# Optimization experiments

Hardware: AMD Instinct MI355X
Metric: run time of the kernel (lower is better)

The kernel has to match this reference:

```python
import jax, jax.numpy as jnp
import numpy as np

NEG_BIG = -9e15

def setup_inputs() -> dict:
    key = jax.random.key(0)
    k1, k2, k3, k4 = jax.random.split(key, 4)
    N, Fin, Fout = 8192, 256, 128
    x = jax.random.normal(k1, (N, Fin), dtype=jnp.float32)
    adj = jax.random.randint(k2, (N, N), 0, 2, dtype=jnp.int32)
    # xavier-uniform-like init
    limW = float(np.sqrt(6.0 / (Fin + Fout)))
    W = jax.random.uniform(k3, (Fin, Fout), minval=-limW, maxval=limW, dtype=jnp.float32)
    lima = float(np.sqrt(6.0 / (2 * Fout + 1)))
    a = jax.random.uniform(k4, (2 * Fout, 1), minval=-lima, maxval=lima, dtype=jnp.float32)
    return {"x": x, "adj": adj, "W": W, "a": a}

def reference(x, adj, W, a, alpha=0.2):
    # h: (N, Fout)
    h = x @ W
    Fout = W.shape[1]
    # Split a into source/target halves: e[i,j] = leakyrelu(h_i·a1 + h_j·a2)
    a1, a2 = a[:Fout, 0], a[Fout:, 0]
    s = h @ a1  # (N,) row (source) scores
    t = h @ a2  # (N,) col (target) scores
    e = jax.nn.leaky_relu(s[:, None] + t[None, :], negative_slope=alpha)  # (N, N)
    e = jnp.where(adj > 0, e, NEG_BIG)
    attention = jax.nn.softmax(e, axis=1)
    # dropout omitted (eval mode / training=False)
    return attention @ h
```

## Files before the change

### kernel.cpp

```cpp
#include <hip/hip_runtime.h>
#include <hip/hip_bf16.h>

typedef __attribute__((ext_vector_type(8))) short short8;
typedef __attribute__((ext_vector_type(4))) short short4v;
typedef __attribute__((ext_vector_type(4))) float f32x4;

#define NR 8192
#define LOG2E 1.4426950408889634f

__device__ __forceinline__ short f2bf(float f) {
  return __builtin_bit_cast(short, __float2bfloat16(f));
}
__device__ __forceinline__ float bf2f(short s) {
  unsigned u = ((unsigned)(unsigned short)s) << 16;
  return __builtin_bit_cast(float, u);
}

__global__ __launch_bounds__(256) void k_gemm_h(const float* __restrict__ x,
                                                const float* __restrict__ W,
                                                short* __restrict__ HT) {
  __shared__ short WT[128][136];
  const int tid = threadIdx.x;
  const int w = tid >> 6;
  const int L = tid & 63;
  const int lm = L & 15;
  const int q = L >> 4;
  const int i0 = blockIdx.x * 128;

  f32x4 acc[2][8];
#pragma unroll
  for (int mm = 0; mm < 2; ++mm)
#pragma unroll
    for (int nn = 0; nn < 8; ++nn) acc[mm][nn] = (f32x4){0.f, 0.f, 0.f, 0.f};

  for (int kc = 0; kc < 256; kc += 128) {
    if (kc) __syncthreads();
#pragma unroll
    for (int p = 0; p < 16; ++p) {
      int idx = p * 256 + tid;
      int k = idx >> 5;
      int f4 = (idx & 31) * 4;
      float4 v = *(const float4*)&W[(kc + k) * 128 + f4];
      WT[f4 + 0][k] = f2bf(v.x);
      WT[f4 + 1][k] = f2bf(v.y);
      WT[f4 + 2][k] = f2bf(v.z);
      WT[f4 + 3][k] = f2bf(v.w);
    }
    __syncthreads();
#pragma unroll
    for (int ks = 0; ks < 4; ++ks) {
      short8 afrag[2];
#pragma unroll
      for (int mm = 0; mm < 2; ++mm) {
        int row = i0 + 32 * w + 16 * mm + lm;
        const float* xp = &x[(size_t)row * 256 + kc + ks * 32 + q * 8];
        float4 xa = *(const float4*)xp;
        float4 xb = *(const float4*)(xp + 4);
        short8 af;
        af[0] = f2bf(xa.x); af[1] = f2bf(xa.y); af[2] = f2bf(xa.z); af[3] = f2bf(xa.w);
        af[4] = f2bf(xb.x); af[5] = f2bf(xb.y); af[6] = f2bf(xb.z); af[7] = f2bf(xb.w);
        afrag[mm] = af;
      }
#pragma unroll
      for (int nn = 0; nn < 8; ++nn) {
        short8 bf = *(const short8*)&WT[nn * 16 + lm][ks * 32 + q * 8];
        acc[0][nn] = __builtin_amdgcn_mfma_f32_16x16x32_bf16(afrag[0], bf, acc[0][nn], 0, 0, 0);
        acc[1][nn] = __builtin_amdgcn_mfma_f32_16x16x32_bf16(afrag[1], bf, acc[1][nn], 0, 0, 0);
      }
    }
  }
#pragma unroll
  for (int mm = 0; mm < 2; ++mm) {
    int ib = i0 + 32 * w + 16 * mm + 4 * q;
#pragma unroll
    for (int nn = 0; nn < 8; ++nn) {
      int f = nn * 16 + lm;
      short4v o;
      o[0] = f2bf(acc[mm][nn][0]);
      o[1] = f2bf(acc[mm][nn][1]);
      o[2] = f2bf(acc[mm][nn][2]);
      o[3] = f2bf(acc[mm][nn][3]);
      *(short4v*)&HT[(size_t)f * NR + ib] = o;
    }
  }
}

__global__ __launch_bounds__(256) void k_st(const short* __restrict__ HT,
                                            const float* __restrict__ a,
                                            float* __restrict__ sv,
                                            float* __restrict__ tv) {
  int i = blockIdx.x * 256 + threadIdx.x;
  float s = 0.f, t = 0.f;
#pragma unroll 4
  for (int f = 0; f < 128; ++f) {
    float h = bf2f(HT[(size_t)f * NR + i]);
    s += h * a[f];
    t += h * a[128 + f];
  }
  sv[i] = s * LOG2E;
  tv[i] = t * LOG2E;
}

__global__ __launch_bounds__(256) void k_flash(const int* __restrict__ adj,
                                               const short* __restrict__ HT,
                                               const float* __restrict__ sv,
                                               const float* __restrict__ tv,
                                               float* __restrict__ part,
                                               float* __restrict__ lpart,
                                               int S, int JR) {
  __shared__ short Ht[128][136];
  const int tid = threadIdx.x;
  const int w = tid >> 6;
  const int L = tid & 63;
  const int lm = L & 15;
  const int q = L >> 4;
  const int sp = blockIdx.x >> 6;
  const int it = blockIdx.x & 63;
  const int i0 = it * 128;

  const int row0 = i0 + 32 * w + lm;
  const int row1 = row0 + 16;
  const float s0 = sv[row0];
  const float s1 = sv[row1];

  f32x4 acc[2][8];
#pragma unroll
  for (int mm = 0; mm < 2; ++mm)
#pragma unroll
    for (int nn = 0; nn < 8; ++nn) acc[mm][nn] = (f32x4){0.f, 0.f, 0.f, 0.f};
  float l0 = 0.f, l1 = 0.f;

  const int ntiles = JR >> 7;
  for (int jt = 0; jt < ntiles; ++jt) {
    const int j0 = sp * JR + jt * 128;
    __syncthreads();
#pragma unroll
    for (int c = 0; c < 8; ++c) {
      int idx = c * 256 + tid;
      int f = idx >> 4;
      int ch = idx & 15;
      *(uint4*)&Ht[f][ch * 8] = *(const uint4*)&HT[(size_t)f * NR + j0 + ch * 8];
    }
    __syncthreads();
#pragma unroll
    for (int kk = 0; kk < 4; ++kk) {
      const int jb = j0 + kk * 32 + q * 8;
      float4 t0 = *(const float4*)&tv[jb];
      float4 t1 = *(const float4*)&tv[jb + 4];
      const int4* ap0 = (const int4*)&adj[(size_t)row0 * NR + jb];
      const int4* ap1 = (const int4*)&adj[(size_t)row1 * NR + jb];
      int4 a00 = ap0[0], a01 = ap0[1];
      int4 a10 = ap1[0], a11 = ap1[1];
      float tvl[8] = {t0.x, t0.y, t0.z, t0.w, t1.x, t1.y, t1.z, t1.w};
      int av0[8] = {a00.x, a00.y, a00.z, a00.w, a01.x, a01.y, a01.z, a01.w};
      int av1[8] = {a10.x, a10.y, a10.z, a10.w, a11.x, a11.y, a11.z, a11.w};
      short8 p0, p1;
#pragma unroll
      for (int e = 0; e < 8; ++e) {
        float v0 = s0 + tvl[e];
        float e0 = fmaxf(v0, 0.2f * v0);
        float pp0 = (av0[e] > 0) ? __builtin_amdgcn_exp2f(e0) : 0.f;
        l0 += pp0;
        p0[e] = f2bf(pp0);
        float v1 = s1 + tvl[e];
        float e1 = fmaxf(v1, 0.2f * v1);
        float pp1 = (av1[e] > 0) ? __builtin_amdgcn_exp2f(e1) : 0.f;
        l1 += pp1;
        p1[e] = f2bf(pp1);
      }
#pragma unroll
      for (int nn = 0; nn < 8; ++nn) {
        short8 bf = *(const short8*)&Ht[nn * 16 + lm][kk * 32 + q * 8];
        acc[0][nn] = __builtin_amdgcn_mfma_f32_16x16x32_bf16(p0, bf, acc[0][nn], 0, 0, 0);
        acc[1][nn] = __builtin_amdgcn_mfma_f32_16x16x32_bf16(p1, bf, acc[1][nn], 0, 0, 0);
      }
    }
  }

  float* ps = part + (size_t)sp * (NR * 128);
#pragma unroll
  for (int mm = 0; mm < 2; ++mm) {
    int ib = i0 + 32 * w + 16 * mm + 4 * q;
#pragma unroll
    for (int nn = 0; nn < 8; ++nn) {
      int f = nn * 16 + lm;
#pragma unroll
      for (int r = 0; r < 4; ++r) ps[(size_t)(ib + r) * 128 + f] = acc[mm][nn][r];
    }
  }
  l0 += __shfl_xor(l0, 16);
  l0 += __shfl_xor(l0, 32);
  l1 += __shfl_xor(l1, 16);
  l1 += __shfl_xor(l1, 32);
  if (q == 0) {
    lpart[sp * NR + row0] = l0;
    lpart[sp * NR + row1] = l1;
  }
}

__global__ __launch_bounds__(256) void k_reduce(const float* __restrict__ part,
                                                const float* __restrict__ lpart,
                                                float* __restrict__ out, int S) {
  int idx = blockIdx.x * 256 + threadIdx.x;
  int i = idx >> 7;
  float sum = 0.f;
  for (int sp = 0; sp < S; ++sp) sum += part[(size_t)sp * (NR * 128) + idx];
  float l = 0.f;
  for (int sp = 0; sp < S; ++sp) l += lpart[sp * NR + i];
  out[idx] = (l > 0.f) ? sum / l : 0.f;
}

extern "C" void kernel_launch(void* const* d_in, const int* in_sizes, int n_in,
                              void* d_out, int out_size, void* d_ws, size_t ws_size,
                              hipStream_t stream) {
  const float* x = (const float*)d_in[0];
  const int* adj = (const int*)d_in[1];
  const float* W = (const float*)d_in[2];
  const float* a = (const float*)d_in[3];
  float* out = (float*)d_out;

  char* ws = (char*)d_ws;
  short* HT = (short*)(ws + 0);
  float* sv = (float*)(ws + 2097152);
  float* tv = (float*)(ws + 2129920);
  float* lpart = (float*)(ws + 2162688);
  float* part = (float*)(ws + 2424832);

  int S = 8;
  while (S > 1 && (size_t)2424832 + (size_t)S * 4194304 > ws_size) S >>= 1;
  int JR = NR / S;

  hipLaunchKernelGGL(k_gemm_h, dim3(64), dim3(256), 0, stream, x, W, HT);
  hipLaunchKernelGGL(k_st, dim3(32), dim3(256), 0, stream, HT, a, sv, tv);
  hipLaunchKernelGGL(k_flash, dim3(64 * S), dim3(256), 0, stream, adj, HT, sv, tv,
                     part, lpart, S, JR);
  hipLaunchKernelGGL(k_reduce, dim3((NR * 128) / 256), dim3(256), 0, stream, part,
                     lpart, out, S);
}
```

Measured before the change: 466.0 us.

## Fuse score computation into GEMM, drop LDS staging in flash, widen split

The s/t score reduction moves into the h GEMM epilogue using cross-lane shuffles, which removes the separate k_st kernel. The GEMM now uses 64-row blocks so the grid is twice as large. The flash kernel stops staging H tiles in LDS behind barriers and loads B fragments straight from global/L2 in a 32-column loop, with launch bounds set for 3 blocks per SM. The split-K factor rises to 16 for more parallelism, and the reduce kernel is vectorised to float4. The trade-offs are more global-load traffic per wave for H and a larger partial buffer to reduce.

```diff
diff --git a/kernel.cpp b/kernel.cpp
--- a/kernel.cpp
+++ b/kernel.cpp
@@ -11,27 +11,24 @@
 __device__ __forceinline__ short f2bf(float f) {
   return __builtin_bit_cast(short, __float2bfloat16(f));
 }
-__device__ __forceinline__ float bf2f(short s) {
-  unsigned u = ((unsigned)(unsigned short)s) << 16;
-  return __builtin_bit_cast(float, u);
-}
 
 __global__ __launch_bounds__(256) void k_gemm_h(const float* __restrict__ x,
                                                 const float* __restrict__ W,
-                                                short* __restrict__ HT) {
+                                                const float* __restrict__ a,
+                                                short* __restrict__ HT,
+                                                float* __restrict__ sv,
+                                                float* __restrict__ tv) {
   __shared__ short WT[128][136];
   const int tid = threadIdx.x;
   const int w = tid >> 6;
   const int L = tid & 63;
   const int lm = L & 15;
   const int q = L >> 4;
-  const int i0 = blockIdx.x * 128;
-
-  f32x4 acc[2][8];
-#pragma unroll
-  for (int mm = 0; mm < 2; ++mm)
-#pragma unroll
-    for (int nn = 0; nn < 8; ++nn) acc[mm][nn] = (f32x4){0.f, 0.f, 0.f, 0.f};
+  const int i0 = blockIdx.x * 64;
+
+  f32x4 acc[8];
+#pragma unroll
+  for (int nn = 0; nn < 8; ++nn) acc[nn] = (f32x4){0.f, 0.f, 0.f, 0.f};
 
   for (int kc = 0; kc < 256; kc += 128) {
     if (kc) __syncthreads();
@@ -49,66 +46,69 @@
     __syncthreads();
 #pragma unroll
     for (int ks = 0; ks < 4; ++ks) {
-      short8 afrag[2];
-#pragma unroll
-      for (int mm = 0; mm < 2; ++mm) {
-        int row = i0 + 32 * w + 16 * mm + lm;
-        const float* xp = &x[(size_t)row * 256 + kc + ks * 32 + q * 8];
-        float4 xa = *(const float4*)xp;
-        float4 xb = *(const float4*)(xp + 4);
-        short8 af;
-        af[0] = f2bf(xa.x); af[1] = f2bf(xa.y); af[2] = f2bf(xa.z); af[3] = f2bf(xa.w);
-        af[4] = f2bf(xb.x); af[5] = f2bf(xb.y); af[6] = f2bf(xb.z); af[7] = f2bf(xb.w);
-        afrag[mm] = af;
-      }
+      int row = i0 + 16 * w + lm;
+      const float* xp = &x[(size_t)row * 256 + kc + ks * 32 + q * 8];
+      float4 xa = *(const float4*)xp;
+      float4 xb = *(const float4*)(xp + 4);
+      short8 af;
+      af[0] = f2bf(xa.x); af[1] = f2bf(xa.y); af[2] = f2bf(xa.z); af[3] = f2bf(xa.w);
+      af[4] = f2bf(xb.x); af[5] = f2bf(xb.y); af[6] = f2bf(xb.z); af[7] = f2bf(xb.w);
 #pragma unroll
       for (int nn = 0; nn < 8; ++nn) {
         short8 bf = *(const short8*)&WT[nn * 16 + lm][ks * 32 + q * 8];
-        acc[0][nn] = __builtin_amdgcn_mfma_f32_16x16x32_bf16(afrag[0], bf, acc[0][nn], 0, 0, 0);
-        acc[1][nn] = __builtin_amdgcn_mfma_f32_16x16x32_bf16(afrag[1], bf, acc[1][nn], 0, 0, 0);
+        acc[nn] = __builtin_amdgcn_mfma_f32_16x16x32_bf16(af, bf, acc[nn], 0, 0, 0);
       }
     }
   }
-#pragma unroll
-  for (int mm = 0; mm < 2; ++mm) {
-    int ib = i0 + 32 * w + 16 * mm + 4 * q;
-#pragma unroll
-    for (int nn = 0; nn < 8; ++nn) {
-      int f = nn * 16 + lm;
-      short4v o;
-      o[0] = f2bf(acc[mm][nn][0]);
-      o[1] = f2bf(acc[mm][nn][1]);
-      o[2] = f2bf(acc[mm][nn][2]);
-      o[3] = f2bf(acc[mm][nn][3]);
-      *(short4v*)&HT[(size_t)f * NR + ib] = o;
-    }
-  }
-}
-
-__global__ __launch_bounds__(256) void k_st(const short* __restrict__ HT,
-                                            const float* __restrict__ a,
-                                            float* __restrict__ sv,
-                                            float* __restrict__ tv) {
-  int i = blockIdx.x * 256 + threadIdx.x;
-  float s = 0.f, t = 0.f;
-#pragma unroll 4
-  for (int f = 0; f < 128; ++f) {
-    float h = bf2f(HT[(size_t)f * NR + i]);
-    s += h * a[f];
-    t += h * a[128 + f];
-  }
-  sv[i] = s * LOG2E;
-  tv[i] = t * LOG2E;
-}
-
-__global__ __launch_bounds__(256) void k_flash(const int* __restrict__ adj,
-                                               const short* __restrict__ HT,
-                                               const float* __restrict__ sv,
-                                               const float* __restrict__ tv,
-                                               float* __restrict__ part,
-                                               float* __restrict__ lpart,
-                                               int S, int JR) {
-  __shared__ short Ht[128][136];
+
+  const int ib = i0 + 16 * w + 4 * q;
+  float a1v[8], a2v[8];
+#pragma unroll
+  for (int nn = 0; nn < 8; ++nn) {
+    a1v[nn] = a[nn * 16 + lm];
+    a2v[nn] = a[128 + nn * 16 + lm];
+  }
+  float sr[4] = {0.f, 0.f, 0.f, 0.f};
+  float tr[4] = {0.f, 0.f, 0.f, 0.f};
+#pragma unroll
+  for (int nn = 0; nn < 8; ++nn) {
+    int f = nn * 16 + lm;
+    short4v o;
+    o[0] = f2bf(acc[nn][0]);
+    o[1] = f2bf(acc[nn][1]);
+    o[2] = f2bf(acc[nn][2]);
+    o[3] = f2bf(acc[nn][3]);
+    *(short4v*)&HT[(size_t)f * NR + ib] = o;
+#pragma unroll
+    for (int r = 0; r < 4; ++r) {
+      sr[r] += acc[nn][r] * a1v[nn];
+      tr[r] += acc[nn][r] * a2v[nn];
+    }
+  }
+#pragma unroll
+  for (int d = 1; d < 16; d <<= 1) {
+#pragma unroll
+    for (int r = 0; r < 4; ++r) {
+      sr[r] += __shfl_xor(sr[r], d);
+      tr[r] += __shfl_xor(tr[r], d);
+    }
+  }
+  if (lm == 0) {
+#pragma unroll
+    for (int r = 0; r < 4; ++r) {
+      sv[ib + r] = sr[r] * LOG2E;
+      tv[ib + r] = tr[r] * LOG2E;
+    }
+  }
+}
+
+__global__ __launch_bounds__(256, 3) void k_flash(const int* __restrict__ adj,
+                                                  const short* __restrict__ HT,
+                                                  const float* __restrict__ sv,
+                                                  const float* __restrict__ tv,
+                                                  float* __restrict__ part,
+                                                  float* __restrict__ lpart,
+                                                  int S) {
   const int tid = threadIdx.x;
   const int w = tid >> 6;
   const int L = tid & 63;
@@ -122,6 +122,8 @@
   const int row1 = row0 + 16;
   const float s0 = sv[row0];
   const float s1 = sv[row1];
+  const size_t ar0 = (size_t)row0 * NR;
+  const size_t ar1 = (size_t)row1 * NR;
 
   f32x4 acc[2][8];
 #pragma unroll
@@ -130,50 +132,45 @@
     for (int nn = 0; nn < 8; ++nn) acc[mm][nn] = (f32x4){0.f, 0.f, 0.f, 0.f};
   float l0 = 0.f, l1 = 0.f;
 
-  const int ntiles = JR >> 7;
-  for (int jt = 0; jt < ntiles; ++jt) {
-    const int j0 = sp * JR + jt * 128;
-    __syncthreads();
-#pragma unroll
-    for (int c = 0; c < 8; ++c) {
-      int idx = c * 256 + tid;
-      int f = idx >> 4;
-      int ch = idx & 15;
-      *(uint4*)&Ht[f][ch * 8] = *(const uint4*)&HT[(size_t)f * NR + j0 + ch * 8];
-    }
-    __syncthreads();
-#pragma unroll
-    for (int kk = 0; kk < 4; ++kk) {
-      const int jb = j0 + kk * 32 + q * 8;
-      float4 t0 = *(const float4*)&tv[jb];
-      float4 t1 = *(const float4*)&tv[jb + 4];
-      const int4* ap0 = (const int4*)&adj[(size_t)row0 * NR + jb];
-      const int4* ap1 = (const int4*)&adj[(size_t)row1 * NR + jb];
-      int4 a00 = ap0[0], a01 = ap0[1];
-      int4 a10 = ap1[0], a11 = ap1[1];
-      float tvl[8] = {t0.x, t0.y, t0.z, t0.w, t1.x, t1.y, t1.z, t1.w};
-      int av0[8] = {a00.x, a00.y, a00.z, a00.w, a01.x, a01.y, a01.z, a01.w};
-      int av1[8] = {a10.x, a10.y, a10.z, a10.w, a11.x, a11.y, a11.z, a11.w};
-      short8 p0, p1;
-#pragma unroll
-      for (int e = 0; e < 8; ++e) {
-        float v0 = s0 + tvl[e];
-        float e0 = fmaxf(v0, 0.2f * v0);
-        float pp0 = (av0[e] > 0) ? __builtin_amdgcn_exp2f(e0) : 0.f;
-        l0 += pp0;
-        p0[e] = f2bf(pp0);
-        float v1 = s1 + tvl[e];
-        float e1 = fmaxf(v1, 0.2f * v1);
-        float pp1 = (av1[e] > 0) ? __builtin_amdgcn_exp2f(e1) : 0.f;
-        l1 += pp1;
-        p1[e] = f2bf(pp1);
-      }
-#pragma unroll
-      for (int nn = 0; nn < 8; ++nn) {
-        short8 bf = *(const short8*)&Ht[nn * 16 + lm][kk * 32 + q * 8];
-        acc[0][nn] = __builtin_amdgcn_mfma_f32_16x16x32_bf16(p0, bf, acc[0][nn], 0, 0, 0);
-        acc[1][nn] = __builtin_amdgcn_mfma_f32_16x16x32_bf16(p1, bf, acc[1][nn], 0, 0, 0);
-      }
+  const int JR = NR / S;
+  const int j0 = sp * JR;
+  const int niter = JR >> 5;
+
+#pragma unroll 2
+  for (int jk = 0; jk < niter; ++jk) {
+    const int jb = j0 + (jk << 5) + q * 8;
+    float4 t0 = *(const float4*)&tv[jb];
+    float4 t1 = *(const float4*)&tv[jb + 4];
+    int4 a00 = *(const int4*)&adj[ar0 + jb];
+    int4 a01 = *(const int4*)&adj[ar0 + jb + 4];
+    int4 a10 = *(const int4*)&adj[ar1 + jb];
+    int4 a11 = *(const int4*)&adj[ar1 + jb + 4];
+    short8 bf[8];
+#pragma unroll
+    for (int nn = 0; nn < 8; ++nn)
+      bf[nn] = *(const short8*)&HT[(size_t)(nn * 16 + lm) * NR + jb];
+
+    float tvl[8] = {t0.x, t0.y, t0.z, t0.w, t1.x, t1.y, t1.z, t1.w};
+    int av0[8] = {a00.x, a00.y, a00.z, a00.w, a01.x, a01.y, a01.z, a01.w};
+    int av1[8] = {a10.x, a10.y, a10.z, a10.w, a11.x, a11.y, a11.z, a11.w};
+    short8 p0, p1;
+#pragma unroll
+    for (int e = 0; e < 8; ++e) {
+      float v0 = s0 + tvl[e];
+      float e0 = fmaxf(v0, 0.2f * v0);
+      float pp0 = (av0[e] > 0) ? __builtin_amdgcn_exp2f(e0) : 0.f;
+      l0 += pp0;
+      p0[e] = f2bf(pp0);
+      float v1 = s1 + tvl[e];
+      float e1 = fmaxf(v1, 0.2f * v1);
+      float pp1 = (av1[e] > 0) ? __builtin_amdgcn_exp2f(e1) : 0.f;
+      l1 += pp1;
+      p1[e] = f2bf(pp1);
+    }
+#pragma unroll
+    for (int nn = 0; nn < 8; ++nn) {
+      acc[0][nn] = __builtin_amdgcn_mfma_f32_16x16x32_bf16(p0, bf[nn], acc[0][nn], 0, 0, 0);
+      acc[1][nn] = __builtin_amdgcn_mfma_f32_16x16x32_bf16(p1, bf[nn], acc[1][nn], 0, 0, 0);
     }
   }
 
@@ -201,13 +198,19 @@
 __global__ __launch_bounds__(256) void k_reduce(const float* __restrict__ part,
                                                 const float* __restrict__ lpart,
                                                 float* __restrict__ out, int S) {
-  int idx = blockIdx.x * 256 + threadIdx.x;
+  int idx4 = blockIdx.x * 256 + threadIdx.x;
+  int idx = idx4 * 4;
   int i = idx >> 7;
-  float sum = 0.f;
-  for (int sp = 0; sp < S; ++sp) sum += part[(size_t)sp * (NR * 128) + idx];
+  float4 sum = {0.f, 0.f, 0.f, 0.f};
+  for (int sp = 0; sp < S; ++sp) {
+    float4 v = *(const float4*)&part[(size_t)sp * (NR * 128) + idx];
+    sum.x += v.x; sum.y += v.y; sum.z += v.z; sum.w += v.w;
+  }
   float l = 0.f;
   for (int sp = 0; sp < S; ++sp) l += lpart[sp * NR + i];
-  out[idx] = (l > 0.f) ? sum / l : 0.f;
+  float inv = (l > 0.f) ? 1.f / l : 0.f;
+  float4 o = {sum.x * inv, sum.y * inv, sum.z * inv, sum.w * inv};
+  *(float4*)&out[idx] = o;
 }
 
 extern "C" void kernel_launch(void* const* d_in, const int* in_sizes, int n_in,
@@ -224,16 +227,14 @@
   float* sv = (float*)(ws + 2097152);
   float* tv = (float*)(ws + 2129920);
   float* lpart = (float*)(ws + 2162688);
-  float* part = (float*)(ws + 2424832);
-
-  int S = 8;
-  while (S > 1 && (size_t)2424832 + (size_t)S * 4194304 > ws_size) S >>= 1;
-  int JR = NR / S;
-
-  hipLaunchKernelGGL(k_gemm_h, dim3(64), dim3(256), 0, stream, x, W, HT);
-  hipLaunchKernelGGL(k_st, dim3(32), dim3(256), 0, stream, HT, a, sv, tv);
+  float* part = (float*)(ws + 3145728);
+
+  int S = 16;
+  while (S > 1 && (size_t)3145728 + (size_t)S * 4194304 > ws_size) S >>= 1;
+
+  hipLaunchKernelGGL(k_gemm_h, dim3(128), dim3(256), 0, stream, x, W, a, HT, sv, tv);
   hipLaunchKernelGGL(k_flash, dim3(64 * S), dim3(256), 0, stream, adj, HT, sv, tv,
-                     part, lpart, S, JR);
-  hipLaunchKernelGGL(k_reduce, dim3((NR * 128) / 256), dim3(256), 0, stream, part,
+                     part, lpart, S);
+  hipLaunchKernelGGL(k_reduce, dim3((NR * 128) / 1024), dim3(256), 0, stream, part,
                      lpart, out, S);
 }
```

Result: faster. 450.3 us (-3.4%).
